# Performance work log

Measured on AMD Instinct MI355X. Metric: run time of the kernel, lower is better.

The kernel has to match this reference:

```python
import jax, jax.numpy as jnp
import numpy as np

B, LP, LE, D, H, DK, DV, DF = 16, 2047, 2048, 1024, 16, 64, 64, 4096


def _layer_norm(x, g, b, eps=1e-5):
    m = x.mean(-1, keepdims=True)
    v = ((x - m) ** 2).mean(-1, keepdims=True)
    return (x - m) * jax.lax.rsqrt(v + eps) * g + b


def _mha(q, kv, wq, wk, wv, wo, bo, g, b):
    # q: [B,Q,D], kv: [B,L,D]; per-head projections wq/wk: [H,D,DK], wv: [H,D,DV]
    residual = q
    Q = jnp.einsum('bqd,hdk->bhqk', q, wq)
    K = jnp.einsum('bld,hdk->bhlk', kv, wk)
    V = jnp.einsum('bld,hdv->bhlv', kv, wv)
    scale = jnp.sqrt(jnp.asarray(Q.shape[-1], Q.dtype))
    attn = jax.nn.softmax(jnp.einsum('bhqk,bhlk->bhql', Q, K) / scale, axis=-1)
    o = jnp.einsum('bhql,bhlv->bhqv', attn, V)
    o = o.transpose(0, 2, 1, 3).reshape(q.shape[0], q.shape[1], -1)  # concat heads
    o = o @ wo + bo
    return _layer_norm(o + residual, g, b), attn


def setup_inputs() -> dict:
    key = jax.random.key(0)
    ks = jax.random.split(key, 16)
    s = 0.02
    inp = {
        'dec_input': jax.random.normal(ks[0], (B, 1, D), jnp.float32),
        'input_history': jax.random.normal(ks[1], (B, LP, D), jnp.float32),
        'enc_output': jax.random.normal(ks[2], (B, LE, D), jnp.float32),
        'wq_s': jax.random.normal(ks[3], (H, D, DK), jnp.float32) * s,
        'wk_s': jax.random.normal(ks[4], (H, D, DK), jnp.float32) * s,
        'wv_s': jax.random.normal(ks[5], (H, D, DV), jnp.float32) * s,
        'wo_s': jax.random.normal(ks[6], (H * DV, D), jnp.float32) * s,
        'bo_s': jnp.zeros((D,), jnp.float32),
        'ln1_g': jnp.ones((D,), jnp.float32),
        'ln1_b': jnp.zeros((D,), jnp.float32),
        'wq_c': jax.random.normal(ks[7], (H, D, DK), jnp.float32) * s,
        'wk_c': jax.random.normal(ks[8], (H, D, DK), jnp.float32) * s,
        'wv_c': jax.random.normal(ks[9], (H, D, DV), jnp.float32) * s,
        'wo_c': jax.random.normal(ks[10], (H * DV, D), jnp.float32) * s,
        'bo_c': jnp.zeros((D,), jnp.float32),
        'ln2_g': jnp.ones((D,), jnp.float32),
        'ln2_b': jnp.zeros((D,), jnp.float32),
        'ffn_w1': jax.random.normal(ks[11], (D, DF), jnp.float32) * s,
        'ffn_b1': jnp.zeros((DF,), jnp.float32),
        'ffn_w2': jax.random.normal(ks[12], (DF, D), jnp.float32) * s,
        'ffn_b2': jnp.zeros((D,), jnp.float32),
        'ln3_g': jnp.ones((D,), jnp.float32),
        'ln3_b': jnp.zeros((D,), jnp.float32),
    }
    return inp


def reference(dec_input, input_history, enc_output,
              wq_s, wk_s, wv_s, wo_s, bo_s, ln1_g, ln1_b,
              wq_c, wk_c, wv_c, wo_c, bo_c, ln2_g, ln2_b,
              ffn_w1, ffn_b1, ffn_w2, ffn_b2, ln3_g, ln3_b):
    # KV-cache growth: history <- cat(history, dec_input)
    history = jnp.concatenate([input_history, dec_input], axis=1)  # [B, LP+1, D]
    x, slf_attn = _mha(dec_input, history, wq_s, wk_s, wv_s, wo_s, bo_s, ln1_g, ln1_b)
    x, enc_attn = _mha(x, enc_output, wq_c, wk_c, wv_c, wo_c, bo_c, ln2_g, ln2_b)
    y = jax.nn.relu(x @ ffn_w1 + ffn_b1) @ ffn_w2 + ffn_b2
    out = _layer_norm(y + x, ln3_g, ln3_b)
    return (out, slf_attn, enc_attn)
```

## Files before the change

kernel.cpp:

```cpp
#include <hip/hip_runtime.h>
#include <hip/hip_bf16.h>
#include <stdint.h>
#include <stddef.h>


#define DEV __device__ __forceinline__

typedef __attribute__((ext_vector_type(8))) short bf16x8;
typedef __attribute__((ext_vector_type(4))) short bf16x4;
typedef __attribute__((ext_vector_type(4))) float f32x4;

DEV unsigned short f2b(float f){
  union { __hip_bfloat16 h; unsigned short u; } cv;
  cv.h = __float2bfloat16(f);
  return cv.u;
}
DEV float b2f(unsigned short u){
  union { unsigned int i; float f; } cv;
  cv.i = ((unsigned int)u) << 16;
  return cv.f;
}
DEV f32x4 mfma16(bf16x8 a, bf16x8 b, f32x4 c){
  return __builtin_amdgcn_mfma_f32_16x16x32_bf16(a, b, c, 0, 0, 0);
}

__global__ __launch_bounds__(256) void g_qp2(const float* __restrict__ src,
    const float* __restrict__ wq, const float* __restrict__ wk,
    unsigned short* __restrict__ qpb){
  int u = blockIdx.x, b = u >> 4, h = u & 15;
  int t = threadIdx.x;
  __shared__ float red[256];
  __shared__ float Qs[64];
  {
    int k = t & 63, q = t >> 6;
    const float* s = src + (size_t)b*1024 + q*256;
    const float* w = wq + (size_t)h*65536 + (size_t)(q*256)*64 + k;
    float a0=0.f,a1=0.f,a2=0.f,a3=0.f;
    for(int d=0; d<256; d+=4){
      a0 += s[d]   * w[(size_t)d*64];
      a1 += s[d+1] * w[(size_t)(d+1)*64];
      a2 += s[d+2] * w[(size_t)(d+2)*64];
      a3 += s[d+3] * w[(size_t)(d+3)*64];
    }
    red[t] = a0+a1+a2+a3;
    __syncthreads();
    if(t < 64) Qs[t] = (red[t]+red[t+64]+red[t+128]+red[t+192])*0.125f;
    __syncthreads();
  }
  for(int i=0;i<4;++i){
    int d = t + i*256;
    const float* w = wk + ((size_t)h*1024 + d)*64;
    float acc = 0.f;
    #pragma unroll
    for(int k4=0;k4<16;++k4){
      float4 wv4 = *(const float4*)(w + k4*4);
      acc += wv4.x*Qs[k4*4] + wv4.y*Qs[k4*4+1] + wv4.z*Qs[k4*4+2] + wv4.w*Qs[k4*4+3];
    }
    qpb[(size_t)u*1024 + d] = f2b(acc);
  }
}

__global__ __launch_bounds__(256) void g_attn(const float* __restrict__ kvsrc,
    const float* __restrict__ decrow, const unsigned short* __restrict__ qpb,
    float* __restrict__ scr, unsigned short* __restrict__ partb,
    float* __restrict__ msum, int lsrc){
  int u = blockIdx.x, ns = u & 63, b = u >> 6;
  int t = threadIdx.x, lane = t & 63, w = t >> 6;
  int r = lane & 15, hi = lane >> 4;
  int slice0 = ns*32;

  __shared__ unsigned short lt[1024*20];
  __shared__ float red[1024];
  __shared__ unsigned short p_lds[16*40];
  __shared__ float f_lds[16];

  float4 ld[16];
  auto ISSUE = [&](int c){
    int row = slice0 + c*16 + r;
    const float* rpp = (row < lsrc) ? kvsrc + ((size_t)b*lsrc + row)*1024
                                    : decrow + (size_t)b*1024;
    rpp += w*256 + hi*8;
    #pragma unroll
    for(int kk=0; kk<8; ++kk){
      ld[kk*2+0] = *(const float4*)(rpp + kk*32);
      ld[kk*2+1] = *(const float4*)(rpp + kk*32 + 4);
    }
  };

  ISSUE(0);
  for(int i=t; i<16*40; i+=256) p_lds[i] = 0;

  bf16x8 qf[8];
  {
    const unsigned short* qp = qpb + ((size_t)b*16 + r)*1024 + w*256 + hi*8;
    #pragma unroll
    for(int kk=0;kk<8;++kk) qf[kk] = *(const bf16x8*)(qp + kk*32);
  }

  f32x4 acc[16];
  #pragma unroll
  for(int i=0;i<16;++i) acc[i] = (f32x4){0.f,0.f,0.f,0.f};
  float m_run = -1e30f, s_run = 0.f;

  __syncthreads();
  for(int c=0; c<2; ++c){
    f32x4 s_acc = {0.f,0.f,0.f,0.f};
    int colw = r ^ ((hi & 1) << 3);
    #pragma unroll
    for(int kk=0; kk<8; ++kk){
      float4 a0 = ld[kk*2], a1 = ld[kk*2+1];
      bf16x8 v;
      v[0]=(short)f2b(a0.x); v[1]=(short)f2b(a0.y);
      v[2]=(short)f2b(a0.z); v[3]=(short)f2b(a0.w);
      v[4]=(short)f2b(a1.x); v[5]=(short)f2b(a1.y);
      v[6]=(short)f2b(a1.z); v[7]=(short)f2b(a1.w);
      unsigned short* pt = &lt[(w*256 + hi*8 + kk*32)*20 + colw];
      #pragma unroll
      for(int j=0;j<8;++j) pt[j*20] = (unsigned short)v[j];
      s_acc = mfma16(v, qf[kk], s_acc);
    }
    if(c < 1) ISSUE(c+1);
    *(f32x4*)&red[t*4] = s_acc;
    __syncthreads();

    f32x4 ss = *(const f32x4*)&red[(0*64+lane)*4];
    ss += *(const f32x4*)&red[(1*64+lane)*4];
    ss += *(const f32x4*)&red[(2*64+lane)*4];
    ss += *(const f32x4*)&red[(3*64+lane)*4];
    float sf[4] = {ss[0], ss[1], ss[2], ss[3]};
    float mc = fmaxf(fmaxf(sf[0],sf[1]), fmaxf(sf[2],sf[3]));
    mc = fmaxf(mc, __shfl_xor(mc, 16));
    mc = fmaxf(mc, __shfl_xor(mc, 32));
    float nm = fmaxf(m_run, mc);
    float fch = __expf(m_run - nm);
    float pvv[4]; float ps = 0.f;
    #pragma unroll
    for(int i=0;i<4;++i){ pvv[i] = __expf(sf[i]-nm); ps += pvv[i]; }
    ps += __shfl_xor(ps, 16);
    ps += __shfl_xor(ps, 32);
    s_run = s_run*fch + ps;
    m_run = nm;
    if(w == 0){
      #pragma unroll
      for(int i=0;i<4;++i) p_lds[r*40 + hi*4 + i] = f2b(pvv[i]);
      if(hi == 0) f_lds[r] = fch;
      float* sp = scr + ((size_t)b*16 + r)*2048 + slice0 + c*16 + hi*4;
      *(float4*)sp = (float4){sf[0], sf[1], sf[2], sf[3]};
    }
    __syncthreads();

    f32x4 fv = *(const f32x4*)&f_lds[hi*4];
    bf16x8 pa = *(const bf16x8*)&p_lds[r*40 + hi*8];
    #pragma unroll
    for(int dc=0; dc<16; ++dc){
      acc[dc] *= fv;
      int d = w*256 + dc*16 + r;
      int col0 = (((hi & 1) ^ ((r >> 3) & 1)) << 3);
      bf16x4 blo = *(const bf16x4*)&lt[d*20 + col0];
      bf16x4 bhi = *(const bf16x4*)&lt[d*20 + col0 + 4];
      bf16x8 bv;
      bv[0]=blo[0]; bv[1]=blo[1]; bv[2]=blo[2]; bv[3]=blo[3];
      bv[4]=bhi[0]; bv[5]=bhi[1]; bv[6]=bhi[2]; bv[7]=bhi[3];
      acc[dc] = mfma16(pa, bv, acc[dc]);
    }
    __syncthreads();
  }
  unsigned short* pl = lt;
  #pragma unroll
  for(int dc=0; dc<16; ++dc)
    #pragma unroll
    for(int i=0;i<4;++i)
      pl[(hi*4+i)*1024 + w*256 + dc*16 + r] = f2b(acc[dc][i]);
  __syncthreads();
  {
    const uint4* s4 = (const uint4*)pl;
    uint4* d4 = (uint4*)(partb + (((size_t)b*64 + ns)*16)*1024);
    #pragma unroll
    for(int j=0;j<8;++j) d4[t + j*256] = s4[t + j*256];
  }
  if(w==0 && hi==0){
    msum[(((size_t)b*64 + ns)*16 + r)*2 + 0] = m_run;
    msum[(((size_t)b*64 + ns)*16 + r)*2 + 1] = s_run;
  }
}

__global__ __launch_bounds__(256) void g_comb(const float* __restrict__ msum,
    const float* __restrict__ scr, const unsigned short* __restrict__ partb,
    float* __restrict__ attn_out, unsigned short* __restrict__ ctxb){
  int dq = blockIdx.x, bh = blockIdx.y, b = bh >> 4, h = bh & 15;
  int t = threadIdx.x;
  __shared__ float e_lds[64];
  __shared__ float Mi[2];
  if(t < 64){
    float2 ms = *(const float2*)&msum[(((size_t)b*64 + t)*16 + h)*2];
    float M = ms.x;
    #pragma unroll
    for(int o=1; o<64; o<<=1) M = fmaxf(M, __shfl_xor(M, o));
    float e = __expf(ms.x - M)*ms.y;
    float S = e;
    #pragma unroll
    for(int o=1; o<64; o<<=1) S += __shfl_xor(S, o);
    e_lds[t] = __expf(ms.x - M)/S;
    if(t == 0){ Mi[0] = M; Mi[1] = 1.f/S; }
  }
  __syncthreads();
  float M = Mi[0], inv = Mi[1];
  const float* sp = scr + (size_t)bh*2048 + dq*512;
  float* po = attn_out + (size_t)bh*2048 + dq*512;
  po[t]     = __expf(sp[t]     - M)*inv;
  po[t+256] = __expf(sp[t+256] - M)*inv;
  int d = dq*256 + t;
  const unsigned short* pb0 = partb + ((size_t)b*64*16 + h)*1024 + d;
  float acc = 0.f;
  #pragma unroll 8
  for(int ns=0; ns<64; ++ns)
    acc += e_lds[ns]*b2f(pb0[(size_t)ns*16384]);
  ctxb[(size_t)bh*1024 + d] = f2b(acc);
}

__global__ __launch_bounds__(256) void g_vproj(const float* __restrict__ wv,
    const unsigned short* __restrict__ ctxb, float* __restrict__ opart){
  int ks = blockIdx.x, h = blockIdx.y;
  int k0b = ks*128;
  __shared__ unsigned short lt[2][64*40];
  int t = threadIdx.x, lane = t & 63, w = t >> 6;
  int k_loc = t >> 3, n_off = (t & 7)*8;
  const unsigned short* apb = ctxb + (size_t)(lane & 15)*16384 + (size_t)h*1024
                              + (lane >> 4)*8 + k0b;
  const float* Wb = wv + (size_t)h*65536;
  f32x4 acc = {0.f,0.f,0.f,0.f};
  float4 x0, x1;
  auto LD = [&](int c){
    const float* wp = Wb + (size_t)(k0b + c*32 + k_loc)*64 + n_off;
    x0 = *(const float4*)wp;
    x1 = *(const float4*)(wp + 4);
  };
  auto ST = [&](int buf){
    unsigned short* p = &lt[buf][0];
    p[(n_off+0)*40 + k_loc] = f2b(x0.x);
    p[(n_off+1)*40 + k_loc] = f2b(x0.y);
    p[(n_off+2)*40 + k_loc] = f2b(x0.z);
    p[(n_off+3)*40 + k_loc] = f2b(x0.w);
    p[(n_off+4)*40 + k_loc] = f2b(x1.x);
    p[(n_off+5)*40 + k_loc] = f2b(x1.y);
    p[(n_off+6)*40 + k_loc] = f2b(x1.z);
    p[(n_off+7)*40 + k_loc] = f2b(x1.w);
  };
  LD(0); ST(0);
  for(int c=0; c<4; ++c){
    if(c+1 < 4) LD(c+1);
    __syncthreads();
    bf16x8 af = *(const bf16x8*)(apb + c*32);
    bf16x8 bv = *(const bf16x8*)&lt[c&1][(w*16 + (lane & 15))*40 + (lane >> 4)*8];
    acc = mfma16(af, bv, acc);
    if(c+1 < 4) ST((c+1)&1);
  }
  int col = w*16 + (lane & 15);
  int r0 = (lane >> 4)*4;
  #pragma unroll
  for(int i=0;i<4;++i)
    opart[ ((size_t)(h*8 + ks)*16 + r0 + i)*64 + col ] = acc[i];
}

__global__ __launch_bounds__(256) void g_ovred(const float* __restrict__ opart,
    unsigned short* __restrict__ ob){
  int i = blockIdx.x*256 + threadIdx.x;
  int b = i >> 10, hv = i & 1023, h = hv >> 6, v = hv & 63;
  float s = 0.f;
  #pragma unroll
  for(int ks=0; ks<8; ++ks)
    s += opart[ ((size_t)(h*8 + ks)*16 + b)*64 + v ];
  ob[(size_t)b*1024 + hv] = f2b(s);
}

__global__ __launch_bounds__(256) void g_ln(const float* __restrict__ parts, int KS,
    const float* __restrict__ bias, const float* __restrict__ resid,
    const float* __restrict__ g, const float* __restrict__ bb,
    float* __restrict__ xout, unsigned short* __restrict__ xb16){
  int b = blockIdx.x, t = threadIdx.x;
  __shared__ float red[256];
  const float4* bias4  = (const float4*)bias;
  const float4* resid4 = (const float4*)resid + (size_t)b*256;
  const float4* parts4 = (const float4*)parts;
  float4 s = bias4[t];
  { float4 rr = resid4[t]; s.x+=rr.x; s.y+=rr.y; s.z+=rr.z; s.w+=rr.w; }
  #pragma unroll 4
  for(int k=0;k<KS;++k){
    float4 pp = parts4[((size_t)k*16 + b)*256 + t];
    s.x+=pp.x; s.y+=pp.y; s.z+=pp.z; s.w+=pp.w;
  }
  red[t] = s.x+s.y+s.z+s.w; __syncthreads();
  for(int off=128; off>0; off>>=1){ if(t<off) red[t]+=red[t+off]; __syncthreads(); }
  float mean = red[0]*(1.f/1024.f); __syncthreads();
  float dx=s.x-mean, dy=s.y-mean, dz=s.z-mean, dw=s.w-mean;
  red[t] = dx*dx+dy*dy+dz*dz+dw*dw; __syncthreads();
  for(int off=128; off>0; off>>=1){ if(t<off) red[t]+=red[t+off]; __syncthreads(); }
  float rstd = rsqrtf(red[0]*(1.f/1024.f) + 1e-5f);
  float4 g4 = ((const float4*)g)[t], b4 = ((const float4*)bb)[t];
  float4 y;
  y.x = dx*rstd*g4.x + b4.x;
  y.y = dy*rstd*g4.y + b4.y;
  y.z = dz*rstd*g4.z + b4.z;
  y.w = dw*rstd*g4.w + b4.w;
  if(xout) ((float4*)xout)[(size_t)b*256 + t] = y;
  if(xb16){
    ushort4 uu;
    uu.x = f2b(y.x); uu.y = f2b(y.y); uu.z = f2b(y.z); uu.w = f2b(y.w);
    ((ushort4*)xb16)[(size_t)b*256 + t] = uu;
  }
}

__global__ __launch_bounds__(256) void g_skg(const float* __restrict__ W,
    const unsigned short* __restrict__ A, float* __restrict__ part,
    int N, int K, int KS){
  int nt = blockIdx.x, ks = blockIdx.y;
  int Ksl = K / KS, k0b = ks * Ksl, n0 = nt*64;
  int nc = Ksl >> 5;
  __shared__ unsigned short lt[2][64*40];
  int t = threadIdx.x, lane = t & 63, w = t >> 6;
  int k_loc = t >> 3, n_off = (t & 7)*8;
  const unsigned short* apb = A + (size_t)(lane & 15)*K + (lane >> 4)*8 + k0b;
  f32x4 acc = {0.f,0.f,0.f,0.f};
  float4 x0, x1;
  auto LD = [&](int c){
    const float* wp = W + (size_t)(k0b + c*32 + k_loc)*N + n0 + n_off;
    x0 = *(const float4*)wp;
    x1 = *(const float4*)(wp + 4);
  };
  auto ST = [&](int buf){
    unsigned short* p = &lt[buf][0];
    p[(n_off+0)*40 + k_loc] = f2b(x0.x);
    p[(n_off+1)*40 + k_loc] = f2b(x0.y);
    p[(n_off+2)*40 + k_loc] = f2b(x0.z);
    p[(n_off+3)*40 + k_loc] = f2b(x0.w);
    p[(n_off+4)*40 + k_loc] = f2b(x1.x);
    p[(n_off+5)*40 + k_loc] = f2b(x1.y);
    p[(n_off+6)*40 + k_loc] = f2b(x1.z);
    p[(n_off+7)*40 + k_loc] = f2b(x1.w);
  };
  LD(0); ST(0);
  for(int c=0; c<nc; ++c){
    if(c+1 < nc) LD(c+1);
    __syncthreads();
    bf16x8 af = *(const bf16x8*)(apb + c*32);
    bf16x8 bv = *(const bf16x8*)&lt[c&1][(w*16 + (lane & 15))*40 + (lane >> 4)*8];
    acc = mfma16(af, bv, acc);
    if(c+1 < nc) ST((c+1)&1);
  }
  int col = n0 + w*16 + (lane & 15);
  int r0 = (lane >> 4)*4;
  #pragma unroll
  for(int i=0;i<4;++i)
    part[ ((size_t)ks*16 + r0 + i)*(size_t)N + col ] = acc[i];
}

__global__ __launch_bounds__(256) void g_relu(const float* __restrict__ parts, int KS,
    const float* __restrict__ b1, unsigned short* __restrict__ h1){
  int i = blockIdx.x*256 + threadIdx.x;
  int b = i >> 10, f4 = i & 1023;
  float4 s = ((const float4*)b1)[f4];
  #pragma unroll 4
  for(int k=0;k<KS;++k){
    float4 pp = ((const float4*)parts)[((size_t)k*16 + b)*1024 + f4];
    s.x+=pp.x; s.y+=pp.y; s.z+=pp.z; s.w+=pp.w;
  }
  ushort4 uu;
  uu.x = f2b(fmaxf(s.x,0.f)); uu.y = f2b(fmaxf(s.y,0.f));
  uu.z = f2b(fmaxf(s.z,0.f)); uu.w = f2b(fmaxf(s.w,0.f));
  ((ushort4*)h1)[i] = uu;
}

extern "C" void kernel_launch(void* const* d_in, const int* in_sizes, int n_in,
                              void* d_out, int out_size, void* d_ws, size_t ws_size,
                              hipStream_t stream){
  const float* dec    = (const float*)d_in[0];
  const float* hist   = (const float*)d_in[1];
  const float* enc    = (const float*)d_in[2];
  const float* wq_s   = (const float*)d_in[3];
  const float* wk_s   = (const float*)d_in[4];
  const float* wv_s   = (const float*)d_in[5];
  const float* wo_s   = (const float*)d_in[6];
  const float* bo_s   = (const float*)d_in[7];
  const float* ln1_g  = (const float*)d_in[8];
  const float* ln1_b  = (const float*)d_in[9];
  const float* wq_c   = (const float*)d_in[10];
  const float* wk_c   = (const float*)d_in[11];
  const float* wv_c   = (const float*)d_in[12];
  const float* wo_c   = (const float*)d_in[13];
  const float* bo_c   = (const float*)d_in[14];
  const float* ln2_g  = (const float*)d_in[15];
  const float* ln2_b  = (const float*)d_in[16];
  const float* w1     = (const float*)d_in[17];
  const float* b1     = (const float*)d_in[18];
  const float* w2     = (const float*)d_in[19];
  const float* b2     = (const float*)d_in[20];
  const float* ln3_g  = (const float*)d_in[21];
  const float* ln3_b  = (const float*)d_in[22];

  float* out  = (float*)d_out;
  float* slf  = out + 16384;
  float* enco = out + 16384 + 524288;

  char* w = (char*)d_ws;
  float*          scr    = (float*)(w + 0x0000000);
  unsigned short* partb  = (unsigned short*)(w + 0x0200000);
  float*          msum   = (float*)(w + 0x2200000);
  unsigned short* qpb    = (unsigned short*)(w + 0x2240000);
  unsigned short* ctxb   = (unsigned short*)(w + 0x22C0000);
  float*          opart  = (float*)(w + 0x2340000);
  unsigned short* ob     = (unsigned short*)(w + 0x23C0000);
  float*          x1     = (float*)(w + 0x23D0000);
  float*          x2     = (float*)(w + 0x23E0000);
  unsigned short* x2b    = (unsigned short*)(w + 0x23F0000);
  unsigned short* h1b    = (unsigned short*)(w + 0x2400000);
  float*          gpart  = (float*)(w + 0x2500000);
  float*          fpart  = (float*)(w + 0x2600000);
  float*          g2part = (float*)(w + 0x2800000);

  g_qp2  <<<256,  256, 0, stream>>>(dec, wq_s, wk_s, qpb);
  g_attn <<<1024, 256, 0, stream>>>(hist, dec, qpb, scr, partb, msum, 2047);
  g_comb <<<dim3(4,256), 256, 0, stream>>>(msum, scr, partb, slf, ctxb);
  g_vproj<<<dim3(8,16),  256, 0, stream>>>(wv_s, ctxb, opart);
  g_ovred<<<64,   256, 0, stream>>>(opart, ob);
  g_skg  <<<dim3(16,16), 256, 0, stream>>>(wo_s, ob, gpart, 1024, 1024, 16);
  g_ln   <<<16,   256, 0, stream>>>(gpart, 16, bo_s, dec, ln1_g, ln1_b, x1, (unsigned short*)0);

  g_qp2  <<<256,  256, 0, stream>>>(x1, wq_c, wk_c, qpb);
  g_attn <<<1024, 256, 0, stream>>>(enc, dec, qpb, scr, partb, msum, 2048);
  g_comb <<<dim3(4,256), 256, 0, stream>>>(msum, scr, partb, enco, ctxb);
  g_vproj<<<dim3(8,16),  256, 0, stream>>>(wv_c, ctxb, opart);
  g_ovred<<<64,   256, 0, stream>>>(opart, ob);
  g_skg  <<<dim3(16,16), 256, 0, stream>>>(wo_c, ob, gpart, 1024, 1024, 16);
  g_ln   <<<16,   256, 0, stream>>>(gpart, 16, bo_c, x1, ln2_g, ln2_b, x2, x2b);

  g_skg  <<<dim3(64,8),  256, 0, stream>>>(w1, x2b, fpart, 4096, 1024, 8);
  g_relu <<<64,  256, 0, stream>>>(fpart, 8, b1, h1b);
  g_skg  <<<dim3(16,32), 256, 0, stream>>>(w2, h1b, g2part, 1024, 4096, 32);
  g_ln   <<<16,  256, 0, stream>>>(g2part, 32, b2, x2, ln3_g, ln3_b, out, (unsigned short*)0);
}
```

Measured before the change: 196.8 us.

## Split Q/K-absorbed projection into MFMA Q GEMM and batched K reduction

Replaces the per-(batch,head) q-projection kernel, which re-read the full per-head wq and wk weights 16 times (once per batch), with two kernels. The first computes Q for all 16 batch rows at once using bf16 MFMA with K-split partials. The second reduces those partials and multiplies by wk with each weight row reused across all batches. This cuts redundant weight traffic at the cost of an extra launch, a partial-sum buffer, and bf16 rounding of the Q computation.

```diff
diff --git a/kernel.cpp b/kernel.cpp
--- a/kernel.cpp
+++ b/kernel.cpp
@@ -24,40 +24,85 @@
   return __builtin_amdgcn_mfma_f32_16x16x32_bf16(a, b, c, 0, 0, 0);
 }
 
-__global__ __launch_bounds__(256) void g_qp2(const float* __restrict__ src,
-    const float* __restrict__ wq, const float* __restrict__ wk,
-    unsigned short* __restrict__ qpb){
-  int u = blockIdx.x, b = u >> 4, h = u & 15;
+__global__ __launch_bounds__(256) void g_qA(const float* __restrict__ src,
+    const float* __restrict__ wq, float* __restrict__ Qpart){
+  int ks = blockIdx.x, h = blockIdx.y;
+  int k0b = ks*128;
+  __shared__ unsigned short lt[2][64*40];
+  int t = threadIdx.x, lane = t & 63, w = t >> 6;
+  int k_loc = t >> 3, n_off = (t & 7)*8;
+  const float* apf = src + (size_t)(lane & 15)*1024 + (lane >> 4)*8 + k0b;
+  const float* Wb = wq + (size_t)h*65536;
+  f32x4 acc = {0.f,0.f,0.f,0.f};
+  float4 x0, x1;
+  auto LD = [&](int c){
+    const float* wp = Wb + (size_t)(k0b + c*32 + k_loc)*64 + n_off;
+    x0 = *(const float4*)wp;
+    x1 = *(const float4*)(wp + 4);
+  };
+  auto ST = [&](int buf){
+    unsigned short* p = &lt[buf][0];
+    p[(n_off+0)*40 + k_loc] = f2b(x0.x);
+    p[(n_off+1)*40 + k_loc] = f2b(x0.y);
+    p[(n_off+2)*40 + k_loc] = f2b(x0.z);
+    p[(n_off+3)*40 + k_loc] = f2b(x0.w);
+    p[(n_off+4)*40 + k_loc] = f2b(x1.x);
+    p[(n_off+5)*40 + k_loc] = f2b(x1.y);
+    p[(n_off+6)*40 + k_loc] = f2b(x1.z);
+    p[(n_off+7)*40 + k_loc] = f2b(x1.w);
+  };
+  LD(0); ST(0);
+  for(int c=0; c<4; ++c){
+    if(c+1 < 4) LD(c+1);
+    __syncthreads();
+    float4 a0 = *(const float4*)(apf + c*32);
+    float4 a1 = *(const float4*)(apf + c*32 + 4);
+    bf16x8 af;
+    af[0]=(short)f2b(a0.x); af[1]=(short)f2b(a0.y);
+    af[2]=(short)f2b(a0.z); af[3]=(short)f2b(a0.w);
+    af[4]=(short)f2b(a1.x); af[5]=(short)f2b(a1.y);
+    af[6]=(short)f2b(a1.z); af[7]=(short)f2b(a1.w);
+    bf16x8 bv = *(const bf16x8*)&lt[c&1][(w*16 + (lane & 15))*40 + (lane >> 4)*8];
+    acc = mfma16(af, bv, acc);
+    if(c+1 < 4) ST((c+1)&1);
+  }
+  int col = w*16 + (lane & 15);
+  int r0 = (lane >> 4)*4;
+  #pragma unroll
+  for(int i=0;i<4;++i)
+    Qpart[ ((size_t)(h*8 + ks)*16 + r0 + i)*64 + col ] = acc[i];
+}
+
+__global__ __launch_bounds__(256) void g_qB(const float* __restrict__ wk,
+    const float* __restrict__ Qpart, unsigned short* __restrict__ qpb){
+  int dt = blockIdx.x, h = blockIdx.y;
   int t = threadIdx.x;
-  __shared__ float red[256];
-  __shared__ float Qs[64];
-  {
-    int k = t & 63, q = t >> 6;
-    const float* s = src + (size_t)b*1024 + q*256;
-    const float* w = wq + (size_t)h*65536 + (size_t)(q*256)*64 + k;
-    float a0=0.f,a1=0.f,a2=0.f,a3=0.f;
-    for(int d=0; d<256; d+=4){
-      a0 += s[d]   * w[(size_t)d*64];
-      a1 += s[d+1] * w[(size_t)(d+1)*64];
-      a2 += s[d+2] * w[(size_t)(d+2)*64];
-      a3 += s[d+3] * w[(size_t)(d+3)*64];
+  __shared__ float Qs[1024];
+  #pragma unroll
+  for(int i=0;i<4;++i){
+    int idx = i*256 + t;
+    float s = 0.f;
+    #pragma unroll
+    for(int ks=0; ks<8; ++ks)
+      s += Qpart[((size_t)h<<13) + (ks<<10) + idx];
+    Qs[idx] = s * 0.125f;
+  }
+  __syncthreads();
+  int d_loc = t & 63, bg = t >> 6;
+  const float* wr = wk + (size_t)h*65536 + (size_t)(dt*64 + d_loc)*64;
+  float acc[4] = {0.f,0.f,0.f,0.f};
+  #pragma unroll
+  for(int k4=0; k4<16; ++k4){
+    float4 w4 = *(const float4*)(wr + k4*4);
+    #pragma unroll
+    for(int i=0;i<4;++i){
+      const float* q = &Qs[(bg*4+i)*64 + k4*4];
+      acc[i] += w4.x*q[0] + w4.y*q[1] + w4.z*q[2] + w4.w*q[3];
     }
-    red[t] = a0+a1+a2+a3;
-    __syncthreads();
-    if(t < 64) Qs[t] = (red[t]+red[t+64]+red[t+128]+red[t+192])*0.125f;
-    __syncthreads();
-  }
-  for(int i=0;i<4;++i){
-    int d = t + i*256;
-    const float* w = wk + ((size_t)h*1024 + d)*64;
-    float acc = 0.f;
-    #pragma unroll
-    for(int k4=0;k4<16;++k4){
-      float4 wv4 = *(const float4*)(w + k4*4);
-      acc += wv4.x*Qs[k4*4] + wv4.y*Qs[k4*4+1] + wv4.z*Qs[k4*4+2] + wv4.w*Qs[k4*4+3];
-    }
-    qpb[(size_t)u*1024 + d] = f2b(acc);
-  }
+  }
+  #pragma unroll
+  for(int i=0;i<4;++i)
+    qpb[ ((size_t)(bg*4+i)*16 + h)*1024 + dt*64 + d_loc ] = f2b(acc[i]);
 }
 
 __global__ __launch_bounds__(256) void g_attn(const float* __restrict__ kvsrc,
@@ -407,17 +452,19 @@
   float*          msum   = (float*)(w + 0x2200000);
   unsigned short* qpb    = (unsigned short*)(w + 0x2240000);
   unsigned short* ctxb   = (unsigned short*)(w + 0x22C0000);
-  float*          opart  = (float*)(w + 0x2340000);
-  unsigned short* ob     = (unsigned short*)(w + 0x23C0000);
-  float*          x1     = (float*)(w + 0x23D0000);
-  float*          x2     = (float*)(w + 0x23E0000);
-  unsigned short* x2b    = (unsigned short*)(w + 0x23F0000);
-  unsigned short* h1b    = (unsigned short*)(w + 0x2400000);
+  float*          Qpart  = (float*)(w + 0x2340000);
+  float*          opart  = (float*)(w + 0x23C0000);
+  unsigned short* ob     = (unsigned short*)(w + 0x2440000);
+  float*          x1     = (float*)(w + 0x2450000);
+  float*          x2     = (float*)(w + 0x2460000);
+  unsigned short* x2b    = (unsigned short*)(w + 0x2470000);
+  unsigned short* h1b    = (unsigned short*)(w + 0x2480000);
   float*          gpart  = (float*)(w + 0x2500000);
   float*          fpart  = (float*)(w + 0x2600000);
   float*          g2part = (float*)(w + 0x2800000);
 
-  g_qp2  <<<256,  256, 0, stream>>>(dec, wq_s, wk_s, qpb);
+  g_qA   <<<dim3(8,16),  256, 0, stream>>>(dec, wq_s, Qpart);
+  g_qB   <<<dim3(16,16), 256, 0, stream>>>(wk_s, Qpart, qpb);
   g_attn <<<1024, 256, 0, stream>>>(hist, dec, qpb, scr, partb, msum, 2047);
   g_comb <<<dim3(4,256), 256, 0, stream>>>(msum, scr, partb, slf, ctxb);
   g_vproj<<<dim3(8,16),  256, 0, stream>>>(wv_s, ctxb, opart);
@@ -425,7 +472,8 @@
   g_skg  <<<dim3(16,16), 256, 0, stream>>>(wo_s, ob, gpart, 1024, 1024, 16);
   g_ln   <<<16,   256, 0, stream>>>(gpart, 16, bo_s, dec, ln1_g, ln1_b, x1, (unsigned short*)0);
 
-  g_qp2  <<<256,  256, 0, stream>>>(x1, wq_c, wk_c, qpb);
+  g_qA   <<<dim3(8,16),  256, 0, stream>>>(x1, wq_c, Qpart);
+  g_qB   <<<dim3(16,16), 256, 0, stream>>>(wk_c, Qpart, qpb);
   g_attn <<<1024, 256, 0, stream>>>(enc, dec, qpb, scr, partb, msum, 2048);
   g_comb <<<dim3(4,256), 256, 0, stream>>>(msum, scr, partb, enco, ctxb);
   g_vproj<<<dim3(8,16),  256, 0, stream>>>(wv_c, ctxb, opart);
```

After: 166.8 us. 1.18x faster.
